# Kernel tuning notes

Measured on AMD Instinct MI355X. Metric: run time of the kernel, lower is better.

The kernel has to match this reference:

```python
import jax, jax.numpy as jnp
import numpy as np

HEAD_SIZE = 64
N_EMBED = 1024
B, T = 8, 2048


def setup_inputs() -> dict:
    key = jax.random.key(0)
    ks = jax.random.split(key, 7)
    s = lambda fan_in: 1.0 / np.sqrt(fan_in)
    return {
        "x": jax.random.normal(ks[0], (B, T, N_EMBED), dtype=jnp.float32),
        # Linear weights stored as (in, out) so projection is x @ W + b
        "Wk": jax.random.uniform(ks[1], (N_EMBED, HEAD_SIZE), jnp.float32, -s(N_EMBED), s(N_EMBED)),
        "bk": jax.random.uniform(ks[2], (HEAD_SIZE,), jnp.float32, -s(N_EMBED), s(N_EMBED)),
        "Wq": jax.random.uniform(ks[3], (N_EMBED, HEAD_SIZE), jnp.float32, -s(N_EMBED), s(N_EMBED)),
        "bq": jax.random.uniform(ks[4], (HEAD_SIZE,), jnp.float32, -s(N_EMBED), s(N_EMBED)),
        "Wv": jax.random.uniform(ks[5], (N_EMBED, HEAD_SIZE), jnp.float32, -s(N_EMBED), s(N_EMBED)),
        "bv": jax.random.uniform(ks[6], (HEAD_SIZE,), jnp.float32, -s(N_EMBED), s(N_EMBED)),
    }


def reference(x, Wk, bk, Wq, bq, Wv, bv):
    Bb, Tt, C = x.shape
    k = x @ Wk + bk  # [B,T,H]
    q = x @ Wq + bq
    v = x @ Wv + bv
    # NOTE: original computes k @ q^T (keys as rows, queries as cols)
    wei = jnp.einsum("bth,bsh->bts", k, q) * (C ** -0.5)  # [B,T,T]
    causal = jnp.tril(jnp.ones((Tt, Tt), dtype=bool))
    wei = jnp.where(causal, wei, -jnp.inf)
    # softplus instead of softmax; softplus(-inf) = 0, stable via logaddexp
    wei = jnp.logaddexp(wei, 0.0)
    # dropout omitted (eval mode / deterministic reference)
    out = jnp.einsum("bts,bsh->bth", wei, v)  # [B,T,H]
    return out
```

## Files before the change

### kernel.cpp

```cpp
#include <hip/hip_runtime.h>
#include <hip/hip_bf16.h>
#include <stdint.h>

#define HEAD 64
#define CEMB 1024
#define BB 8
#define TSEQ 2048
#define PBK 64

typedef __attribute__((ext_vector_type(8))) short bf16x8;
typedef __attribute__((ext_vector_type(4))) float f32x4;

__device__ __forceinline__ unsigned short f2bf(float f) {
    union { float f; uint32_t u; } c; c.f = f;
    uint32_t u = c.u + 0x7FFF + ((c.u >> 16) & 1);
    return (unsigned short)(u >> 16);
}

__global__ __launch_bounds__(256) void prep_w(
        const float* __restrict__ Wk, const float* __restrict__ bk,
        const float* __restrict__ Wq, const float* __restrict__ bq,
        const float* __restrict__ Wv, const float* __restrict__ bv,
        unsigned short* __restrict__ WT, float* __restrict__ biasb) {
    __shared__ float Ws[64][68];
    const int p = blockIdx.x >> 4, kc = blockIdx.x & 15;
    const float* W  = (p == 0) ? Wk : (p == 1) ? Wq : Wv;
    const float* bi = (p == 0) ? bk : (p == 1) ? bq : bv;
    const float scale = (p == 1) ? 0.03125f : 1.0f;
    const int tid = threadIdx.x;
    const int h4 = (tid & 15) * 4;
    for (int r = 0; r < 4; r++) {
        int kl = (tid >> 4) + r * 16;
        float4 v = *(const float4*)(W + (long)(kc * 64 + kl) * 64 + h4);
        *(float4*)(&Ws[kl][h4]) = v;
    }
    __syncthreads();
    const int h = tid >> 2, k0 = (tid & 3) * 16;
    unsigned short ov[16];
    for (int i = 0; i < 16; i++) ov[i] = f2bf(Ws[k0 + i][h] * scale);
    unsigned short* dst = WT + (long)(p * 64 + h) * CEMB + kc * 64 + k0;
    *(int4*)(dst)     = *(int4*)(ov);
    *(int4*)(dst + 8) = *((int4*)(ov) + 1);
    if (kc == 0 && tid < 64) biasb[p * 64 + tid] = bi[tid] * scale;
}

__global__ __launch_bounds__(256) void proj_gemm(
        const float* __restrict__ x, const unsigned short* __restrict__ WT,
        const float* __restrict__ biasb,
        unsigned short* __restrict__ Kb, unsigned short* __restrict__ Qb,
        unsigned short* __restrict__ VTb) {
    __shared__ __align__(16) unsigned short Bs[2][192 * 72];

    const int tid = threadIdx.x;
    const int lane = tid & 63, w = tid >> 6;
    const int l15 = lane & 15, q4 = lane >> 4;
    const int mw = w & 1, nw = w >> 1;
    const long rowbase = (long)blockIdx.x * 32;

    const float* xg = x + (rowbase + mw * 16 + l15) * CEMB + q4 * 8;

    f32x4 z = {0.f, 0.f, 0.f, 0.f};
    f32x4 acc[6];
    for (int j = 0; j < 6; j++) acc[j] = z;

    float4 apf[4];
    int4   bpf[6];

    for (int kk = 0; kk < 2; kk++)
        for (int c = 0; c < 2; c++)
            apf[kk * 2 + c] = *(const float4*)(xg + kk * 32 + c * 4);
    for (int i = 0; i < 6; i++) {
        int c = i * 256 + tid, n = c >> 3, kc = c & 7;
        bpf[i] = *(const int4*)(WT + (long)n * CEMB + kc * 8);
    }
    for (int i = 0; i < 6; i++) {
        int c = i * 256 + tid, n = c >> 3, kc = c & 7;
        *(int4*)(&Bs[0][n * 72 + kc * 8]) = bpf[i];
    }
    __syncthreads();

    for (int seg = 0; seg < 16; seg++) {
        const int cur = seg & 1;
        bf16x8 af[2];
        for (int kk = 0; kk < 2; kk++) {
            unsigned short t8[8];
            const float* f = (const float*)&apf[kk * 2];
            for (int e = 0; e < 8; e++) t8[e] = f2bf(f[e]);
            af[kk] = *(bf16x8*)t8;
        }
        if (seg < 15) {
            const float* xs = xg + (seg + 1) * PBK;
            for (int kk = 0; kk < 2; kk++)
                for (int c = 0; c < 2; c++)
                    apf[kk * 2 + c] = *(const float4*)(xs + kk * 32 + c * 4);
            for (int i = 0; i < 6; i++) {
                int c = i * 256 + tid, n = c >> 3, kc = c & 7;
                bpf[i] = *(const int4*)(WT + (long)n * CEMB + (seg + 1) * PBK + kc * 8);
            }
        }
        for (int kk = 0; kk < 2; kk++)
            for (int j = 0; j < 6; j++) {
                bf16x8 bf = *(const bf16x8*)(
                    &Bs[cur][(nw * 96 + j * 16 + l15) * 72 + kk * 32 + q4 * 8]);
                acc[j] = __builtin_amdgcn_mfma_f32_16x16x32_bf16(af[kk], bf, acc[j], 0, 0, 0);
            }
        if (seg < 15) {
            for (int i = 0; i < 6; i++) {
                int c = i * 256 + tid, n = c >> 3, kc = c & 7;
                *(int4*)(&Bs[cur ^ 1][n * 72 + kc * 8]) = bpf[i];
            }
        }
        __syncthreads();
    }

    for (int j = 0; j < 6; j++) {
        const int n = nw * 96 + j * 16 + l15;
        const float bias = biasb[n];
        const long row0 = rowbase + mw * 16 + q4 * 4;
        if (n < 128) {
            unsigned short* dst = (n < 64) ? (Kb + row0 * HEAD + n)
                                           : (Qb + row0 * HEAD + (n - 64));
            for (int r = 0; r < 4; r++)
                dst[r * HEAD] = f2bf(acc[j][r] + bias);
        } else {
            const int h = n - 128;
            const long b = row0 >> 11; const int t = (int)(row0 & 2047);
            ushort4 pk;
            pk.x = f2bf(acc[j][0] + bias);
            pk.y = f2bf(acc[j][1] + bias);
            pk.z = f2bf(acc[j][2] + bias);
            pk.w = f2bf(acc[j][3] + bias);
            *(ushort4*)(VTb + b * (HEAD * (long)TSEQ) + (long)h * TSEQ + t) = pk;
        }
    }
}

__global__ __launch_bounds__(256) void attn(
        const unsigned short* __restrict__ Kb, const unsigned short* __restrict__ Qb,
        const unsigned short* __restrict__ VTb, float* __restrict__ out) {
    __shared__ __align__(16) unsigned short Pl[4][16 * 40];
    __shared__ __align__(16) float red[3][64 * 20];

    const int tid = threadIdx.x;
    const int lane = tid & 63, w = tid >> 6;
    const int l15 = lane & 15, q4 = lane >> 4;

    const int bid = blockIdx.x;
    const int ti = 127 - (bid >> 3);
    const int b = bid & 7;
    const int t0 = ti * 16;

    const unsigned short* kb  = Kb  + (long)b * TSEQ * HEAD;
    const unsigned short* qb  = Qb  + (long)b * TSEQ * HEAD;
    const unsigned short* vtb = VTb + (long)b * HEAD * TSEQ;

    bf16x8 kf0 = *(const bf16x8*)(kb + (t0 + l15) * HEAD + q4 * 8);
    bf16x8 kf1 = *(const bf16x8*)(kb + (t0 + l15) * HEAD + 32 + q4 * 8);

    f32x4 z = {0.f, 0.f, 0.f, 0.f};
    f32x4 oacc[4] = {z, z, z, z};

    unsigned short* myP = &Pl[w][0];
    const int nchunk = (t0 + 15) / 32 + 1;

    for (int c = w; c < nchunk; c += 4) {
        const int s0 = c * 32;
        f32x4 st[2];
        for (int tile = 0; tile < 2; tile++) {
            int sb = s0 + tile * 16;
            bf16x8 qf0 = *(const bf16x8*)(qb + (sb + l15) * HEAD + q4 * 8);
            bf16x8 qf1 = *(const bf16x8*)(qb + (sb + l15) * HEAD + 32 + q4 * 8);
            f32x4 sc = z;
            sc = __builtin_amdgcn_mfma_f32_16x16x32_bf16(qf0, kf0, sc, 0, 0, 0);
            sc = __builtin_amdgcn_mfma_f32_16x16x32_bf16(qf1, kf1, sc, 0, 0, 0);
            st[tile] = sc;
        }
        const int tg = t0 + l15;
        for (int tile = 0; tile < 2; tile++) {
            ushort4 pk;
            unsigned short pv[4];
            for (int r = 0; r < 4; r++) {
                int sg = s0 + tile * 16 + q4 * 4 + r;
                float p = __logf(1.0f + __expf(st[tile][r]));
                if (sg > tg) p = 0.0f;
                pv[r] = f2bf(p);
            }
            pk.x = pv[0]; pk.y = pv[1]; pk.z = pv[2]; pk.w = pv[3];
            *(ushort4*)(myP + l15 * 40 + tile * 16 + q4 * 4) = pk;
        }
        __threadfence_block();
        bf16x8 pf = *(const bf16x8*)(myP + l15 * 40 + q4 * 8);
        for (int hh = 0; hh < 4; hh++) {
            bf16x8 vf = *(const bf16x8*)(vtb + (hh * 16 + l15) * (long)TSEQ + s0 + q4 * 8);
            oacc[hh] = __builtin_amdgcn_mfma_f32_16x16x32_bf16(vf, pf, oacc[hh], 0, 0, 0);
        }
    }

    if (w > 0) {
        float* r0 = &red[w - 1][lane * 20];
        for (int hh = 0; hh < 4; hh++)
            *(f32x4*)(r0 + hh * 4) = oacc[hh];
    }
    __syncthreads();
    if (w == 0) {
        for (int i = 0; i < 3; i++) {
            const float* r0 = &red[i][lane * 20];
            for (int hh = 0; hh < 4; hh++)
                oacc[hh] += *(const f32x4*)(r0 + hh * 4);
        }
        float* ob = out + ((long)b * TSEQ + t0 + l15) * HEAD + q4 * 4;
        for (int hh = 0; hh < 4; hh++)
            *(f32x4*)(ob + hh * 16) = oacc[hh];
    }
}

extern "C" void kernel_launch(void* const* d_in, const int* in_sizes, int n_in,
                              void* d_out, int out_size, void* d_ws, size_t ws_size,
                              hipStream_t stream) {
    const float* x  = (const float*)d_in[0];
    const float* Wk = (const float*)d_in[1];
    const float* bk = (const float*)d_in[2];
    const float* Wq = (const float*)d_in[3];
    const float* bq = (const float*)d_in[4];
    const float* Wv = (const float*)d_in[5];
    const float* bv = (const float*)d_in[6];
    float* out = (float*)d_out;

    char* ws = (char*)d_ws;
    unsigned short* WT    = (unsigned short*)(ws);
    float*          biasb = (float*)(ws + 393216);
    unsigned short* Kb    = (unsigned short*)(ws + 524288);
    unsigned short* Qb    = (unsigned short*)(ws + 524288 + 2097152);
    unsigned short* VTb   = (unsigned short*)(ws + 524288 + 4194304);

    prep_w<<<48, 256, 0, stream>>>(Wk, bk, Wq, bq, Wv, bv, WT, biasb);
    proj_gemm<<<512, 256, 0, stream>>>(x, WT, biasb, Kb, Qb, VTb);
    attn<<<1024, 256, 0, stream>>>(Kb, Qb, VTb, out);
}
```

Measured before the change: 163.9 us.

## Stage full x row-tile in LDS and double attention query tile to 32

The projection GEMM now loads and converts the entire 32x1024 x tile to bf16 in shared memory once, then streams weight fragments directly from global/L2 instead of double-buffering both operands through LDS with per-segment syncs. The attention kernel processes 32 key rows per block instead of 16, reusing each Q/V fragment load across two tiles and halving the grid to 512 blocks. The aim is to cut global traffic and barriers. In exchange it uses more registers and LDS per block and leaves fewer blocks for load balancing across the causal triangle.

```diff
diff --git a/kernel.cpp b/kernel.cpp
--- a/kernel.cpp
+++ b/kernel.cpp
@@ -6,7 +6,6 @@
 #define CEMB 1024
 #define BB 8
 #define TSEQ 2048
-#define PBK 64
 
 typedef __attribute__((ext_vector_type(8))) short bf16x8;
 typedef __attribute__((ext_vector_type(4))) float f32x4;
@@ -15,6 +14,10 @@
     union { float f; uint32_t u; } c; c.f = f;
     uint32_t u = c.u + 0x7FFF + ((c.u >> 16) & 1);
     return (unsigned short)(u >> 16);
+}
+__device__ __forceinline__ ushort4 f4bf(float4 v) {
+    ushort4 u; u.x = f2bf(v.x); u.y = f2bf(v.y); u.z = f2bf(v.z); u.w = f2bf(v.w);
+    return u;
 }
 
 __global__ __launch_bounds__(256) void prep_w(
@@ -49,7 +52,7 @@
         const float* __restrict__ biasb,
         unsigned short* __restrict__ Kb, unsigned short* __restrict__ Qb,
         unsigned short* __restrict__ VTb) {
-    __shared__ __align__(16) unsigned short Bs[2][192 * 72];
+    __shared__ __align__(16) unsigned short As[32 * 1032];
 
     const int tid = threadIdx.x;
     const int lane = tid & 63, w = tid >> 6;
@@ -57,60 +60,41 @@
     const int mw = w & 1, nw = w >> 1;
     const long rowbase = (long)blockIdx.x * 32;
 
-    const float* xg = x + (rowbase + mw * 16 + l15) * CEMB + q4 * 8;
+    {
+        const int r = tid >> 3, c8 = tid & 7;
+        const float* xr = x + (rowbase + r) * CEMB + c8 * 4;
+        unsigned short* lr = As + r * 1032 + c8 * 4;
+        #pragma unroll
+        for (int i = 0; i < 32; i += 4) {
+            float4 v0 = *(const float4*)(xr + (i + 0) * 32);
+            float4 v1 = *(const float4*)(xr + (i + 1) * 32);
+            float4 v2 = *(const float4*)(xr + (i + 2) * 32);
+            float4 v3 = *(const float4*)(xr + (i + 3) * 32);
+            *(ushort4*)(lr + (i + 0) * 32) = f4bf(v0);
+            *(ushort4*)(lr + (i + 1) * 32) = f4bf(v1);
+            *(ushort4*)(lr + (i + 2) * 32) = f4bf(v2);
+            *(ushort4*)(lr + (i + 3) * 32) = f4bf(v3);
+        }
+    }
+    __syncthreads();
 
     f32x4 z = {0.f, 0.f, 0.f, 0.f};
     f32x4 acc[6];
     for (int j = 0; j < 6; j++) acc[j] = z;
 
-    float4 apf[4];
-    int4   bpf[6];
-
-    for (int kk = 0; kk < 2; kk++)
-        for (int c = 0; c < 2; c++)
-            apf[kk * 2 + c] = *(const float4*)(xg + kk * 32 + c * 4);
-    for (int i = 0; i < 6; i++) {
-        int c = i * 256 + tid, n = c >> 3, kc = c & 7;
-        bpf[i] = *(const int4*)(WT + (long)n * CEMB + kc * 8);
-    }
-    for (int i = 0; i < 6; i++) {
-        int c = i * 256 + tid, n = c >> 3, kc = c & 7;
-        *(int4*)(&Bs[0][n * 72 + kc * 8]) = bpf[i];
-    }
-    __syncthreads();
-
-    for (int seg = 0; seg < 16; seg++) {
-        const int cur = seg & 1;
-        bf16x8 af[2];
-        for (int kk = 0; kk < 2; kk++) {
-            unsigned short t8[8];
-            const float* f = (const float*)&apf[kk * 2];
-            for (int e = 0; e < 8; e++) t8[e] = f2bf(f[e]);
-            af[kk] = *(bf16x8*)t8;
-        }
-        if (seg < 15) {
-            const float* xs = xg + (seg + 1) * PBK;
-            for (int kk = 0; kk < 2; kk++)
-                for (int c = 0; c < 2; c++)
-                    apf[kk * 2 + c] = *(const float4*)(xs + kk * 32 + c * 4);
-            for (int i = 0; i < 6; i++) {
-                int c = i * 256 + tid, n = c >> 3, kc = c & 7;
-                bpf[i] = *(const int4*)(WT + (long)n * CEMB + (seg + 1) * PBK + kc * 8);
-            }
-        }
-        for (int kk = 0; kk < 2; kk++)
-            for (int j = 0; j < 6; j++) {
-                bf16x8 bf = *(const bf16x8*)(
-                    &Bs[cur][(nw * 96 + j * 16 + l15) * 72 + kk * 32 + q4 * 8]);
-                acc[j] = __builtin_amdgcn_mfma_f32_16x16x32_bf16(af[kk], bf, acc[j], 0, 0, 0);
-            }
-        if (seg < 15) {
-            for (int i = 0; i < 6; i++) {
-                int c = i * 256 + tid, n = c >> 3, kc = c & 7;
-                *(int4*)(&Bs[cur ^ 1][n * 72 + kc * 8]) = bpf[i];
-            }
-        }
-        __syncthreads();
+    const unsigned short* Am = As + (mw * 16 + l15) * 1032 + q4 * 8;
+    const unsigned short* Bg = WT + (long)(nw * 96 + l15) * CEMB + q4 * 8;
+
+    #pragma unroll 4
+    for (int kc = 0; kc < 32; kc++) {
+        bf16x8 a = *(const bf16x8*)(Am + kc * 32);
+        bf16x8 bfr[6];
+        #pragma unroll
+        for (int j = 0; j < 6; j++)
+            bfr[j] = *(const bf16x8*)(Bg + (long)j * 16 * CEMB + kc * 32);
+        #pragma unroll
+        for (int j = 0; j < 6; j++)
+            acc[j] = __builtin_amdgcn_mfma_f32_16x16x32_bf16(a, bfr[j], acc[j], 0, 0, 0);
     }
 
     for (int j = 0; j < 6; j++) {
@@ -138,79 +122,92 @@
 __global__ __launch_bounds__(256) void attn(
         const unsigned short* __restrict__ Kb, const unsigned short* __restrict__ Qb,
         const unsigned short* __restrict__ VTb, float* __restrict__ out) {
-    __shared__ __align__(16) unsigned short Pl[4][16 * 40];
-    __shared__ __align__(16) float red[3][64 * 20];
+    __shared__ __align__(16) unsigned short Pl[4][2][32 * 40];
+    __shared__ __align__(16) float red[3][64 * 36];
 
     const int tid = threadIdx.x;
     const int lane = tid & 63, w = tid >> 6;
     const int l15 = lane & 15, q4 = lane >> 4;
 
     const int bid = blockIdx.x;
-    const int ti = 127 - (bid >> 3);
+    const int ti = 63 - (bid >> 3);
     const int b = bid & 7;
-    const int t0 = ti * 16;
+    const int t0 = ti * 32;
 
     const unsigned short* kb  = Kb  + (long)b * TSEQ * HEAD;
     const unsigned short* qb  = Qb  + (long)b * TSEQ * HEAD;
     const unsigned short* vtb = VTb + (long)b * HEAD * TSEQ;
 
-    bf16x8 kf0 = *(const bf16x8*)(kb + (t0 + l15) * HEAD + q4 * 8);
-    bf16x8 kf1 = *(const bf16x8*)(kb + (t0 + l15) * HEAD + 32 + q4 * 8);
+    bf16x8 kf[2][2];
+    for (int tt = 0; tt < 2; tt++)
+        for (int kk = 0; kk < 2; kk++)
+            kf[tt][kk] = *(const bf16x8*)(kb + (t0 + tt * 16 + l15) * HEAD + kk * 32 + q4 * 8);
 
     f32x4 z = {0.f, 0.f, 0.f, 0.f};
-    f32x4 oacc[4] = {z, z, z, z};
-
-    unsigned short* myP = &Pl[w][0];
-    const int nchunk = (t0 + 15) / 32 + 1;
-
-    for (int c = w; c < nchunk; c += 4) {
+    f32x4 oacc[4][2];
+    for (int hh = 0; hh < 4; hh++) for (int tt = 0; tt < 2; tt++) oacc[hh][tt] = z;
+
+    int buf = 0;
+    for (int c = w; c <= ti; c += 4) {
         const int s0 = c * 32;
-        f32x4 st[2];
-        for (int tile = 0; tile < 2; tile++) {
-            int sb = s0 + tile * 16;
-            bf16x8 qf0 = *(const bf16x8*)(qb + (sb + l15) * HEAD + q4 * 8);
-            bf16x8 qf1 = *(const bf16x8*)(qb + (sb + l15) * HEAD + 32 + q4 * 8);
-            f32x4 sc = z;
-            sc = __builtin_amdgcn_mfma_f32_16x16x32_bf16(qf0, kf0, sc, 0, 0, 0);
-            sc = __builtin_amdgcn_mfma_f32_16x16x32_bf16(qf1, kf1, sc, 0, 0, 0);
-            st[tile] = sc;
-        }
-        const int tg = t0 + l15;
-        for (int tile = 0; tile < 2; tile++) {
-            ushort4 pk;
-            unsigned short pv[4];
-            for (int r = 0; r < 4; r++) {
-                int sg = s0 + tile * 16 + q4 * 4 + r;
-                float p = __logf(1.0f + __expf(st[tile][r]));
-                if (sg > tg) p = 0.0f;
-                pv[r] = f2bf(p);
+        unsigned short* myP = &Pl[w][buf][0];
+
+        f32x4 sc[2][2];
+        for (int st2 = 0; st2 < 2; st2++) {
+            bf16x8 qf0 = *(const bf16x8*)(qb + (s0 + st2 * 16 + l15) * HEAD + q4 * 8);
+            bf16x8 qf1 = *(const bf16x8*)(qb + (s0 + st2 * 16 + l15) * HEAD + 32 + q4 * 8);
+            for (int tt = 0; tt < 2; tt++) {
+                f32x4 s = z;
+                s = __builtin_amdgcn_mfma_f32_16x16x32_bf16(qf0, kf[tt][0], s, 0, 0, 0);
+                s = __builtin_amdgcn_mfma_f32_16x16x32_bf16(qf1, kf[tt][1], s, 0, 0, 0);
+                sc[st2][tt] = s;
             }
-            pk.x = pv[0]; pk.y = pv[1]; pk.z = pv[2]; pk.w = pv[3];
-            *(ushort4*)(myP + l15 * 40 + tile * 16 + q4 * 4) = pk;
+        }
+        for (int tt = 0; tt < 2; tt++) {
+            const int tg = t0 + tt * 16 + l15;
+            for (int st2 = 0; st2 < 2; st2++) {
+                ushort4 pk;
+                unsigned short pv[4];
+                for (int r = 0; r < 4; r++) {
+                    int sg = s0 + st2 * 16 + q4 * 4 + r;
+                    float p = __logf(1.0f + __expf(sc[st2][tt][r]));
+                    if (sg > tg) p = 0.0f;
+                    pv[r] = f2bf(p);
+                }
+                pk.x = pv[0]; pk.y = pv[1]; pk.z = pv[2]; pk.w = pv[3];
+                *(ushort4*)(myP + (tt * 16 + l15) * 40 + st2 * 16 + q4 * 4) = pk;
+            }
         }
         __threadfence_block();
-        bf16x8 pf = *(const bf16x8*)(myP + l15 * 40 + q4 * 8);
+        bf16x8 pf0 = *(const bf16x8*)(myP + l15 * 40 + q4 * 8);
+        bf16x8 pf1 = *(const bf16x8*)(myP + (16 + l15) * 40 + q4 * 8);
         for (int hh = 0; hh < 4; hh++) {
             bf16x8 vf = *(const bf16x8*)(vtb + (hh * 16 + l15) * (long)TSEQ + s0 + q4 * 8);
-            oacc[hh] = __builtin_amdgcn_mfma_f32_16x16x32_bf16(vf, pf, oacc[hh], 0, 0, 0);
-        }
+            oacc[hh][0] = __builtin_amdgcn_mfma_f32_16x16x32_bf16(vf, pf0, oacc[hh][0], 0, 0, 0);
+            oacc[hh][1] = __builtin_amdgcn_mfma_f32_16x16x32_bf16(vf, pf1, oacc[hh][1], 0, 0, 0);
+        }
+        buf ^= 1;
     }
 
     if (w > 0) {
-        float* r0 = &red[w - 1][lane * 20];
+        float* r0 = &red[w - 1][lane * 36];
         for (int hh = 0; hh < 4; hh++)
-            *(f32x4*)(r0 + hh * 4) = oacc[hh];
+            for (int tt = 0; tt < 2; tt++)
+                *(f32x4*)(r0 + (hh * 2 + tt) * 4) = oacc[hh][tt];
     }
     __syncthreads();
     if (w == 0) {
         for (int i = 0; i < 3; i++) {
-            const float* r0 = &red[i][lane * 20];
+            const float* r0 = &red[i][lane * 36];
             for (int hh = 0; hh < 4; hh++)
-                oacc[hh] += *(const f32x4*)(r0 + hh * 4);
-        }
-        float* ob = out + ((long)b * TSEQ + t0 + l15) * HEAD + q4 * 4;
-        for (int hh = 0; hh < 4; hh++)
-            *(f32x4*)(ob + hh * 16) = oacc[hh];
+                for (int tt = 0; tt < 2; tt++)
+                    oacc[hh][tt] += *(const f32x4*)(r0 + (hh * 2 + tt) * 4);
+        }
+        for (int tt = 0; tt < 2; tt++) {
+            float* ob = out + ((long)b * TSEQ + t0 + tt * 16 + l15) * HEAD + q4 * 4;
+            for (int hh = 0; hh < 4; hh++)
+                *(f32x4*)(ob + hh * 16) = oacc[hh][tt];
+        }
     }
 }
 
@@ -235,5 +232,5 @@
 
     prep_w<<<48, 256, 0, stream>>>(Wk, bk, Wq, bq, Wv, bv, WT, biasb);
     proj_gemm<<<512, 256, 0, stream>>>(x, WT, biasb, Kb, Qb, VTb);
-    attn<<<1024, 256, 0, stream>>>(Kb, Qb, VTb, out);
-}
+    attn<<<512, 256, 0, stream>>>(Kb, Qb, VTb, out);
+}
```

New measurement: 191.0 us. 1.17x slower.
